# Optimization experiments

Hardware: AMD Instinct MI355X
Metric: run time of the kernel (lower is better)

Reference implementation:

```python
import jax, jax.numpy as jnp
import numpy as np

OUT, IN, GROUP = 4096, 4096, 128
NG = IN // GROUP  # 32 groups along in_features
TOKENS = 8192

def setup_inputs() -> dict:
    key = jax.random.key(0)
    k1, k2, k3, k4, k5 = jax.random.split(key, 5)
    input = jax.random.normal(k1, (TOKENS, IN), dtype=jnp.float32)
    qweight = jax.random.randint(k2, (OUT, IN), 0, 16, dtype=jnp.int32)
    scales = jax.random.uniform(k3, (OUT, NG), dtype=jnp.float32) * 0.02 + 0.001
    zeros = jax.random.uniform(k4, (OUT, NG), dtype=jnp.float32) * 15.0
    bias = jax.random.normal(k5, (OUT,), dtype=jnp.float32)
    return {"input": input, "qweight": qweight, "scales": scales, "zeros": zeros, "bias": bias}

def dequantize(qweight, scales, zeros):
    # qweight: [OUT, IN] int; scales/zeros: [OUT, NG]; group along in_features
    q = qweight.astype(jnp.float32).reshape(OUT, NG, GROUP)
    w = (q - zeros[:, :, None]) * scales[:, :, None]
    return w.reshape(OUT, IN)

def reference(input, qweight, scales, zeros, bias):
    # F.linear(input, W, bias) == input @ W.T + bias
    W = dequantize(qweight, scales, zeros)
    return jnp.einsum('ti,oi->to', input, W) + bias
```

## Files before the change

kernel.cpp:

```cpp
#include <hip/hip_runtime.h>
#include <hip/hip_bf16.h>
#include <cstdint>

typedef __attribute__((ext_vector_type(4))) float  floatx4;
typedef __attribute__((ext_vector_type(8))) __bf16 bf16x8;

#define M_T 8192
#define N_T 4096
#define K_T 4096
#define NG  32

__device__ __forceinline__ unsigned short f2bf(float f) {
    union { float f; unsigned int u; } v; v.f = f;
    unsigned int u = v.u;
    u += 0x7fffu + ((u >> 16) & 1u);
    return (unsigned short)(u >> 16);
}

__device__ __forceinline__ void load_lds16(const void* gsrc, void* ldst) {
    __builtin_amdgcn_global_load_lds(
        (const __attribute__((address_space(1))) uint32_t*)gsrc,
        (__attribute__((address_space(3))) uint32_t*)ldst,
        16, 0, 0);
}

__global__ void dequant_w_kernel(const int* __restrict__ q,
                                 const float* __restrict__ sc,
                                 const float* __restrict__ zr,
                                 unsigned short* __restrict__ Wb) {
    int idx = blockIdx.x * 256 + threadIdx.x;
    int e0 = idx << 2;
    int row = e0 >> 12;
    int col = e0 & 4095;
    int g = col >> 7;
    float s = sc[(row << 5) + g];
    float z = zr[(row << 5) + g];
    int4 qv = *(const int4*)(q + e0);
    ushort4 o;
    o.x = f2bf(((float)qv.x - z) * s);
    o.y = f2bf(((float)qv.y - z) * s);
    o.z = f2bf(((float)qv.z - z) * s);
    o.w = f2bf(((float)qv.w - z) * s);
    *(ushort4*)(Wb + e0) = o;
}

__global__ void convert_x_kernel(const float* __restrict__ X,
                                 unsigned short* __restrict__ Xb) {
    int idx = blockIdx.x * 256 + threadIdx.x;
    int e0 = idx << 2;
    float4 xv = *(const float4*)(X + e0);
    ushort4 o;
    o.x = f2bf(xv.x); o.y = f2bf(xv.y); o.z = f2bf(xv.z); o.w = f2bf(xv.w);
    *(ushort4*)(Xb + e0) = o;
}

__global__ __launch_bounds__(512, 2) void gemm256_8ph(
    const unsigned short* __restrict__ Xb,
    const unsigned short* __restrict__ Wb,
    const float* __restrict__ bias,
    float* __restrict__ C)
{
    __shared__ __align__(16) unsigned short lds[65536];
    char* ldsb = (char*)lds;

    const int tid  = threadIdx.x;
    const int lane = tid & 63;
    const int wid  = tid >> 6;
    const int wm   = wid >> 2;
    const int wn   = wid & 3;

    int bid = blockIdx.x;
    int xcd = bid & 7, r0 = bid >> 3;
    int mt = (xcd >> 1) * 8 + (r0 & 7);
    int nt = (xcd & 1) * 8 + (r0 >> 3);
    const int bm = mt * 256;
    const int bn = nt * 256;

    floatx4 acc[8][4] = {};

    const int klb = (lane >> 4) * 16;

    auto stage_half = [&](int buf, int isB, int half, int grow0, int k0,
                          const unsigned short* __restrict__ G) {
        char* base = ldsb + buf * 65536 + isB * 32768 + half * 16384;
        #pragma unroll
        for (int c = 0; c < 2; ++c) {
            int r  = c * 64 + wid * 8 + (lane >> 3);
            int cb = ((lane & 7) * 16) ^ ((lane >> 3) << 4);
            const char* src = (const char*)(G + (size_t)(grow0 + r) * K_T + k0) + cb;
            load_lds16(src, base + c * 8192 + wid * 1024);
        }
    };
    auto rdA = [&](int buf, int mf, int kb) -> bf16x8 {
        int r = mf * 16 + (lane & 15);
        int off = buf * 65536 + wm * 16384 + r * 128 + (kb ^ ((r & 7) << 4));
        return *(const bf16x8*)(ldsb + off);
    };
    auto rdB = [&](int buf, int nf, int kb) -> bf16x8 {
        int r = (wn & 1) * 64 + nf * 16 + (lane & 15);
        int off = buf * 65536 + 32768 + (wn >> 1) * 16384 + r * 128 + (kb ^ ((r & 7) << 4));
        return *(const bf16x8*)(ldsb + off);
    };

    stage_half(0, 1, 0, bn,       0,  Wb);
    stage_half(0, 1, 1, bn + 128, 0,  Wb);
    stage_half(0, 0, 0, bm,       0,  Xb);
    stage_half(0, 0, 1, bm + 128, 0,  Xb);
    stage_half(1, 1, 0, bn,       64, Wb);
    stage_half(1, 1, 1, bn + 128, 64, Wb);
    asm volatile("s_waitcnt vmcnt(4)" ::: "memory");
    __builtin_amdgcn_s_barrier();

    bf16x8 bfr[4][2];

    for (int t = 0; t < 32; ++t) {
        const int t1 = 2 * t + 1;
        const int t2 = (2 * t + 2 < 64) ? 2 * t + 2 : 63;
        const int t3 = (2 * t + 3 < 64) ? 2 * t + 3 : 63;
        #pragma unroll
        for (int p = 0; p < 8; ++p) {
            const int cb    = p >> 2;
            const int q     = p & 3;
            const int mbase = (q & 1) * 4;
            const int kkp   = q >> 1;

            if (q == 0) {
                #pragma unroll
                for (int nf = 0; nf < 4; ++nf)
                    bfr[nf][0] = rdB(cb, nf, klb);
            }
            if (q == 1) {
                #pragma unroll
                for (int nf = 0; nf < 4; ++nf)
                    bfr[nf][1] = rdB(cb, nf, 64 + klb);
            }
            bf16x8 a[4];
            #pragma unroll
            for (int m = 0; m < 4; ++m)
                a[m] = rdA(cb, mbase + m, kkp * 64 + klb);

            switch (p) {
                case 0: stage_half(1, 0, 0, bm,       t1 * 64, Xb); break;
                case 1: stage_half(1, 0, 1, bm + 128, t1 * 64, Xb); break;
                case 2: stage_half(0, 1, 0, bn,       t2 * 64, Wb); break;
                case 3: stage_half(0, 1, 1, bn + 128, t2 * 64, Wb); break;
                case 4: stage_half(0, 0, 0, bm,       t2 * 64, Xb); break;
                case 5: stage_half(0, 0, 1, bm + 128, t2 * 64, Xb); break;
                case 6: stage_half(1, 1, 0, bn,       t3 * 64, Wb); break;
                case 7: stage_half(1, 1, 1, bn + 128, t3 * 64, Wb); break;
            }

            __builtin_amdgcn_s_barrier();

            __builtin_amdgcn_s_setprio(1);
            #pragma unroll
            for (int m = 0; m < 4; ++m)
                #pragma unroll
                for (int nf = 0; nf < 4; ++nf)
                    acc[mbase + m][nf] = __builtin_amdgcn_mfma_f32_16x16x32_bf16(
                        a[m], bfr[nf][kkp], acc[mbase + m][nf], 0, 0, 0);
            __builtin_amdgcn_s_setprio(0);

            if (q == 1)
                asm volatile("s_waitcnt lgkmcnt(0)" ::: "memory");
            if (q == 3)
                asm volatile("s_waitcnt vmcnt(4)" ::: "memory");
            __builtin_amdgcn_s_barrier();
        }
    }

    asm volatile("s_waitcnt vmcnt(0)" ::: "memory");

    #pragma unroll
    for (int nf = 0; nf < 4; ++nf) {
        int col = bn + wn * 64 + nf * 16 + (lane & 15);
        float bv = bias[col];
        #pragma unroll
        for (int mf = 0; mf < 8; ++mf) {
            int row0 = bm + wm * 128 + mf * 16 + (lane >> 4) * 4;
            #pragma unroll
            for (int j = 0; j < 4; ++j)
                C[(size_t)(row0 + j) * N_T + col] = acc[mf][nf][j] + bv;
        }
    }
}

__global__ void fallback_gemm(const float* __restrict__ X,
                              const int* __restrict__ q,
                              const float* __restrict__ sc,
                              const float* __restrict__ zr,
                              const float* __restrict__ bias,
                              float* __restrict__ C) {
    __shared__ float sX[16][17];
    __shared__ float sW[16][17];
    int tx = threadIdx.x, ty = threadIdx.y;
    int row = blockIdx.y * 16 + ty;
    int col = blockIdx.x * 16 + tx;
    float acc = 0.f;
    for (int k0 = 0; k0 < K_T; k0 += 16) {
        sX[ty][tx] = X[(size_t)row * K_T + k0 + tx];
        int wrow = blockIdx.x * 16 + ty;
        int kc = k0 + tx;
        int g = kc >> 7;
        sW[ty][tx] = ((float)q[(size_t)wrow * K_T + kc] - zr[wrow * NG + g]) * sc[wrow * NG + g];
        __syncthreads();
        #pragma unroll
        for (int kk = 0; kk < 16; ++kk) acc += sX[ty][kk] * sW[tx][kk];
        __syncthreads();
    }
    C[(size_t)row * N_T + col] = acc + bias[col];
}

extern "C" void kernel_launch(void* const* d_in, const int* in_sizes, int n_in,
                              void* d_out, int out_size, void* d_ws, size_t ws_size,
                              hipStream_t stream) {
    const float* input   = (const float*)d_in[0];
    const int*   qweight = (const int*)d_in[1];
    const float* scales  = (const float*)d_in[2];
    const float* zeros   = (const float*)d_in[3];
    const float* bias    = (const float*)d_in[4];
    float* out = (float*)d_out;

    const size_t needW = (size_t)N_T * K_T * sizeof(unsigned short);
    const size_t needX = (size_t)M_T * K_T * sizeof(unsigned short);

    if (ws_size >= needW + needX) {
        unsigned short* Wb = (unsigned short*)d_ws;
        unsigned short* Xb = (unsigned short*)((char*)d_ws + needW);

        dequant_w_kernel<<<(N_T * K_T / 4) / 256, 256, 0, stream>>>(qweight, scales, zeros, Wb);
        convert_x_kernel<<<(M_T * K_T / 4) / 256, 256, 0, stream>>>(input, Xb);

        gemm256_8ph<<<512, 512, 0, stream>>>(Xb, Wb, bias, out);
    } else {
        dim3 blk(16, 16);
        dim3 grid(N_T / 16, M_T / 16);
        fallback_gemm<<<grid, blk, 0, stream>>>(input, qweight, scales, zeros, bias, out);
    }
}
```

Baseline: 284.9 us.

## Prefetch next-phase LDS fragments after MFMAs and drop mid-phase barrier

Precomputes per-lane LDS read offsets and global staging addresses so the inner loop uses constant-offset addressing. Moves the A and second-half B fragment reads to after each MFMA block, so LDS reads for the next phase overlap the current MFMA work. Removes the barrier between staging and compute in each phase, halving barriers per phase. This keeps more fragment registers live, and dropping the barrier relies on the remaining waitcnt and barrier placement still protecting the LDS buffers from being overwritten while in use.

```diff
diff --git a/kernel.cpp b/kernel.cpp
--- a/kernel.cpp
+++ b/kernel.cpp
@@ -78,40 +78,50 @@
 
     floatx4 acc[8][4] = {};
 
-    const int klb = (lane >> 4) * 16;
-
-    auto stage_half = [&](int buf, int isB, int half, int grow0, int k0,
-                          const unsigned short* __restrict__ G) {
-        char* base = ldsb + buf * 65536 + isB * 32768 + half * 16384;
-        #pragma unroll
-        for (int c = 0; c < 2; ++c) {
-            int r  = c * 64 + wid * 8 + (lane >> 3);
-            int cb = ((lane & 7) * 16) ^ ((lane >> 3) << 4);
-            const char* src = (const char*)(G + (size_t)(grow0 + r) * K_T + k0) + cb;
-            load_lds16(src, base + c * 8192 + wid * 1024);
+    const int klb  = (lane >> 4) * 16;
+    const int axor = (lane & 7) << 4;
+
+    int obA[2][2], obB[2][2];
+    #pragma unroll
+    for (int b = 0; b < 2; ++b)
+        #pragma unroll
+        for (int kp = 0; kp < 2; ++kp) {
+            obA[b][kp] = b * 65536 + wm * 16384 + (lane & 15) * 128
+                       + ((kp * 64 + klb) ^ axor);
+            obB[b][kp] = b * 65536 + 32768 + (wn >> 1) * 16384 + (wn & 1) * 8192
+                       + (lane & 15) * 128 + ((kp * 64 + klb) ^ axor);
         }
+
+    auto rA = [&](int b, int kp, int mf) -> bf16x8 {
+        return *(const bf16x8*)(ldsb + obA[b][kp] + mf * 2048);
     };
-    auto rdA = [&](int buf, int mf, int kb) -> bf16x8 {
-        int r = mf * 16 + (lane & 15);
-        int off = buf * 65536 + wm * 16384 + r * 128 + (kb ^ ((r & 7) << 4));
-        return *(const bf16x8*)(ldsb + off);
+    auto rB = [&](int b, int kp, int nf) -> bf16x8 {
+        return *(const bf16x8*)(ldsb + obB[b][kp] + nf * 2048);
     };
-    auto rdB = [&](int buf, int nf, int kb) -> bf16x8 {
-        int r = (wn & 1) * 64 + nf * 16 + (lane & 15);
-        int off = buf * 65536 + 32768 + (wn >> 1) * 16384 + r * 128 + (kb ^ ((r & 7) << 4));
-        return *(const bf16x8*)(ldsb + off);
+
+    const int pl0 = (wid * 8 + (lane >> 3)) * 8192
+                  + (((lane & 7) * 16) ^ ((lane >> 3) << 4));
+    const int pl1 = pl0 + 64 * 8192;
+    const char* GA = (const char*)Xb + (size_t)bm * 8192;
+    const char* GB = (const char*)Wb + (size_t)bn * 8192;
+
+    auto stage_half = [&](int buf, int isB, int half, int tk, const char* G) {
+        char* dst = ldsb + buf * 65536 + isB * 32768 + half * 16384 + wid * 1024;
+        const char* s0 = G + ((size_t)half * 1048576 + (size_t)tk * 128);
+        load_lds16(s0 + pl0, dst);
+        load_lds16(s0 + pl1, dst + 8192);
     };
 
-    stage_half(0, 1, 0, bn,       0,  Wb);
-    stage_half(0, 1, 1, bn + 128, 0,  Wb);
-    stage_half(0, 0, 0, bm,       0,  Xb);
-    stage_half(0, 0, 1, bm + 128, 0,  Xb);
-    stage_half(1, 1, 0, bn,       64, Wb);
-    stage_half(1, 1, 1, bn + 128, 64, Wb);
+    stage_half(0, 1, 0, 0, GB);
+    stage_half(0, 1, 1, 0, GB);
+    stage_half(0, 0, 0, 0, GA);
+    stage_half(0, 0, 1, 0, GA);
+    stage_half(1, 1, 0, 1, GB);
+    stage_half(1, 1, 1, 1, GB);
     asm volatile("s_waitcnt vmcnt(4)" ::: "memory");
     __builtin_amdgcn_s_barrier();
 
-    bf16x8 bfr[4][2];
+    bf16x8 a[4], bfr[4][2];
 
     for (int t = 0; t < 32; ++t) {
         const int t1 = 2 * t + 1;
@@ -121,36 +131,26 @@
         for (int p = 0; p < 8; ++p) {
             const int cb    = p >> 2;
             const int q     = p & 3;
+            const int kkp   = q >> 1;
             const int mbase = (q & 1) * 4;
-            const int kkp   = q >> 1;
 
             if (q == 0) {
                 #pragma unroll
-                for (int nf = 0; nf < 4; ++nf)
-                    bfr[nf][0] = rdB(cb, nf, klb);
-            }
-            if (q == 1) {
-                #pragma unroll
-                for (int nf = 0; nf < 4; ++nf)
-                    bfr[nf][1] = rdB(cb, nf, 64 + klb);
-            }
-            bf16x8 a[4];
-            #pragma unroll
-            for (int m = 0; m < 4; ++m)
-                a[m] = rdA(cb, mbase + m, kkp * 64 + klb);
+                for (int nf = 0; nf < 4; ++nf) bfr[nf][0] = rB(cb, 0, nf);
+                #pragma unroll
+                for (int m = 0; m < 4; ++m)    a[m] = rA(cb, 0, m);
+            }
 
             switch (p) {
-                case 0: stage_half(1, 0, 0, bm,       t1 * 64, Xb); break;
-                case 1: stage_half(1, 0, 1, bm + 128, t1 * 64, Xb); break;
-                case 2: stage_half(0, 1, 0, bn,       t2 * 64, Wb); break;
-                case 3: stage_half(0, 1, 1, bn + 128, t2 * 64, Wb); break;
-                case 4: stage_half(0, 0, 0, bm,       t2 * 64, Xb); break;
-                case 5: stage_half(0, 0, 1, bm + 128, t2 * 64, Xb); break;
-                case 6: stage_half(1, 1, 0, bn,       t3 * 64, Wb); break;
-                case 7: stage_half(1, 1, 1, bn + 128, t3 * 64, Wb); break;
-            }
-
-            __builtin_amdgcn_s_barrier();
+                case 0: stage_half(1, 0, 0, t1, GA); break;
+                case 1: stage_half(1, 0, 1, t1, GA); break;
+                case 2: stage_half(0, 1, 0, t2, GB); break;
+                case 3: stage_half(0, 1, 1, t2, GB); break;
+                case 4: stage_half(0, 0, 0, t2, GA); break;
+                case 5: stage_half(0, 0, 1, t2, GA); break;
+                case 6: stage_half(1, 1, 0, t3, GB); break;
+                case 7: stage_half(1, 1, 1, t3, GB); break;
+            }
 
             __builtin_amdgcn_s_setprio(1);
             #pragma unroll
@@ -160,6 +160,16 @@
                     acc[mbase + m][nf] = __builtin_amdgcn_mfma_f32_16x16x32_bf16(
                         a[m], bfr[nf][kkp], acc[mbase + m][nf], 0, 0, 0);
             __builtin_amdgcn_s_setprio(0);
+
+            if (q == 0) {
+                #pragma unroll
+                for (int nf = 0; nf < 4; ++nf) bfr[nf][1] = rB(cb, 1, nf);
+            }
+            if (q < 3) {
+                const int qn = q + 1, kkn = qn >> 1, mbn = (qn & 1) * 4;
+                #pragma unroll
+                for (int m = 0; m < 4; ++m) a[m] = rA(cb, kkn, mbn + m);
+            }
 
             if (q == 1)
                 asm volatile("s_waitcnt lgkmcnt(0)" ::: "memory");
```

After: 277.5 us. 2.6% less time.

## Restructure GEMM to 256x128 tiles with BK=32 triple-buffered LDS pipeline

Applied to the files above, without the earlier changes.

Replaces the 256x256-tile, 512-thread, BK=64 double-buffered GEMM with a 256x128-tile, 256-thread kernel using K-steps of 32 and a three-slot LDS ring. Loads run two tiles ahead and are split around the two MFMA halves, with a new XOR swizzle for 64-byte rows. The grid doubles to 1024 blocks with a remapped XCD tile assignment. The aim is smaller LDS use and finer-grained overlap of loads and MFMA, at the cost of more barriers per FLOP and more global traffic from the narrower N tile.

```diff
diff --git a/kernel.cpp b/kernel.cpp
--- a/kernel.cpp
+++ b/kernel.cpp
@@ -54,120 +54,111 @@
     *(ushort4*)(Xb + e0) = o;
 }
 
-__global__ __launch_bounds__(512, 2) void gemm256_8ph(
+__global__ __launch_bounds__(256, 2) void gemm_bk32(
     const unsigned short* __restrict__ Xb,
     const unsigned short* __restrict__ Wb,
     const float* __restrict__ bias,
     float* __restrict__ C)
 {
-    __shared__ __align__(16) unsigned short lds[65536];
+    __shared__ __align__(16) unsigned short lds[36864];
     char* ldsb = (char*)lds;
 
     const int tid  = threadIdx.x;
     const int lane = tid & 63;
     const int wid  = tid >> 6;
-    const int wm   = wid >> 2;
-    const int wn   = wid & 3;
+    const int wm   = wid >> 1;
+    const int wn   = wid & 1;
 
     int bid = blockIdx.x;
     int xcd = bid & 7, r0 = bid >> 3;
     int mt = (xcd >> 1) * 8 + (r0 & 7);
-    int nt = (xcd & 1) * 8 + (r0 >> 3);
+    int nt = (xcd & 1) * 16 + (r0 >> 3);
     const int bm = mt * 256;
-    const int bn = nt * 256;
+    const int bn = nt * 128;
 
     floatx4 acc[8][4] = {};
 
-    const int klb = (lane >> 4) * 16;
-
-    auto stage_half = [&](int buf, int isB, int half, int grow0, int k0,
-                          const unsigned short* __restrict__ G) {
-        char* base = ldsb + buf * 65536 + isB * 32768 + half * 16384;
-        #pragma unroll
-        for (int c = 0; c < 2; ++c) {
-            int r  = c * 64 + wid * 8 + (lane >> 3);
-            int cb = ((lane & 7) * 16) ^ ((lane >> 3) << 4);
-            const char* src = (const char*)(G + (size_t)(grow0 + r) * K_T + k0) + cb;
-            load_lds16(src, base + c * 8192 + wid * 1024);
-        }
-    };
-    auto rdA = [&](int buf, int mf, int kb) -> bf16x8 {
-        int r = mf * 16 + (lane & 15);
-        int off = buf * 65536 + wm * 16384 + r * 128 + (kb ^ ((r & 7) << 4));
-        return *(const bf16x8*)(ldsb + off);
-    };
-    auto rdB = [&](int buf, int nf, int kb) -> bf16x8 {
-        int r = (wn & 1) * 64 + nf * 16 + (lane & 15);
-        int off = buf * 65536 + 32768 + (wn >> 1) * 16384 + r * 128 + (kb ^ ((r & 7) << 4));
-        return *(const bf16x8*)(ldsb + off);
-    };
-
-    stage_half(0, 1, 0, bn,       0,  Wb);
-    stage_half(0, 1, 1, bn + 128, 0,  Wb);
-    stage_half(0, 0, 0, bm,       0,  Xb);
-    stage_half(0, 0, 1, bm + 128, 0,  Xb);
-    stage_half(1, 1, 0, bn,       64, Wb);
-    stage_half(1, 1, 1, bn + 128, 64, Wb);
-    asm volatile("s_waitcnt vmcnt(4)" ::: "memory");
+    const int l15 = lane & 15;
+    const int g   = lane >> 4;
+    const int obRead = l15 * 64 + 16 * (g ^ ((l15 >> 1) & 3));
+    const int obA_v  = obRead + wm * 8192;
+    const int obB_v  = 49152 + obRead + wn * 4096;
+
+    auto rA = [&](int sa, int mf) -> bf16x8 {
+        return *(const bf16x8*)(ldsb + obA_v + sa * 16384 + mf * 1024);
+    };
+    auto rB = [&](int sb, int nf) -> bf16x8 {
+        return *(const bf16x8*)(ldsb + obB_v + sb * 8192 + nf * 1024);
+    };
+
+    const int plS = (wid * 16 + (lane >> 2)) * 8192
+                  + 16 * ((lane & 3) ^ ((lane >> 3) & 3));
+    const char* GA = (const char*)Xb + (size_t)bm * 8192;
+    const char* GB = (const char*)Wb + (size_t)bn * 8192;
+
+    auto stA = [&](int slot, int tk, int c) {
+        load_lds16(GA + (size_t)tk * 64 + c * 524288 + plS,
+                   ldsb + slot * 16384 + c * 4096 + wid * 1024);
+    };
+    auto stB = [&](int slot, int tk, int c) {
+        load_lds16(GB + (size_t)tk * 64 + c * 524288 + plS,
+                   ldsb + 49152 + slot * 8192 + c * 4096 + wid * 1024);
+    };
+
+    stB(0, 0, 0); stB(0, 0, 1);
+    stA(0, 0, 0); stA(0, 0, 1); stA(0, 0, 2); stA(0, 0, 3);
+    stB(1, 1, 0); stB(1, 1, 1);
+    stA(1, 1, 0); stA(1, 1, 1); stA(1, 1, 2); stA(1, 1, 3);
+    asm volatile("s_waitcnt vmcnt(6)" ::: "memory");
     __builtin_amdgcn_s_barrier();
-
-    bf16x8 bfr[4][2];
-
-    for (int t = 0; t < 32; ++t) {
-        const int t1 = 2 * t + 1;
-        const int t2 = (2 * t + 2 < 64) ? 2 * t + 2 : 63;
-        const int t3 = (2 * t + 3 < 64) ? 2 * t + 3 : 63;
-        #pragma unroll
-        for (int p = 0; p < 8; ++p) {
-            const int cb    = p >> 2;
-            const int q     = p & 3;
-            const int mbase = (q & 1) * 4;
-            const int kkp   = q >> 1;
-
-            if (q == 0) {
-                #pragma unroll
-                for (int nf = 0; nf < 4; ++nf)
-                    bfr[nf][0] = rdB(cb, nf, klb);
-            }
-            if (q == 1) {
-                #pragma unroll
-                for (int nf = 0; nf < 4; ++nf)
-                    bfr[nf][1] = rdB(cb, nf, 64 + klb);
-            }
-            bf16x8 a[4];
+    asm volatile("" ::: "memory");
+
+    bf16x8 a[4], bfr[4];
+    #pragma unroll
+    for (int nf = 0; nf < 4; ++nf) bfr[nf] = rB(0, nf);
+    #pragma unroll
+    for (int m = 0; m < 4; ++m)    a[m] = rA(0, m);
+
+    auto tile_body = [&](int t, int sa, int sa1, int sa2) {
+        const int tk2 = (t + 2 < 128) ? t + 2 : 127;
+        stB(sa2, tk2, 0); stB(sa2, tk2, 1); stA(sa2, tk2, 0);
+        __builtin_amdgcn_s_setprio(1);
+        #pragma unroll
+        for (int m = 0; m < 4; ++m)
             #pragma unroll
-            for (int m = 0; m < 4; ++m)
-                a[m] = rdA(cb, mbase + m, kkp * 64 + klb);
-
-            switch (p) {
-                case 0: stage_half(1, 0, 0, bm,       t1 * 64, Xb); break;
-                case 1: stage_half(1, 0, 1, bm + 128, t1 * 64, Xb); break;
-                case 2: stage_half(0, 1, 0, bn,       t2 * 64, Wb); break;
-                case 3: stage_half(0, 1, 1, bn + 128, t2 * 64, Wb); break;
-                case 4: stage_half(0, 0, 0, bm,       t2 * 64, Xb); break;
-                case 5: stage_half(0, 0, 1, bm + 128, t2 * 64, Xb); break;
-                case 6: stage_half(1, 1, 0, bn,       t3 * 64, Wb); break;
-                case 7: stage_half(1, 1, 1, bn + 128, t3 * 64, Wb); break;
-            }
-
-            __builtin_amdgcn_s_barrier();
-
-            __builtin_amdgcn_s_setprio(1);
+            for (int nf = 0; nf < 4; ++nf)
+                acc[m][nf] = __builtin_amdgcn_mfma_f32_16x16x32_bf16(
+                    a[m], bfr[nf], acc[m][nf], 0, 0, 0);
+        __builtin_amdgcn_s_setprio(0);
+        #pragma unroll
+        for (int m = 0; m < 4; ++m) a[m] = rA(sa, 4 + m);
+        asm volatile("s_waitcnt vmcnt(3)" ::: "memory");
+        __builtin_amdgcn_s_barrier();
+        asm volatile("" ::: "memory");
+        stA(sa2, tk2, 1); stA(sa2, tk2, 2); stA(sa2, tk2, 3);
+        __builtin_amdgcn_s_setprio(1);
+        #pragma unroll
+        for (int m = 0; m < 4; ++m)
             #pragma unroll
-            for (int m = 0; m < 4; ++m)
-                #pragma unroll
-                for (int nf = 0; nf < 4; ++nf)
-                    acc[mbase + m][nf] = __builtin_amdgcn_mfma_f32_16x16x32_bf16(
-                        a[m], bfr[nf][kkp], acc[mbase + m][nf], 0, 0, 0);
-            __builtin_amdgcn_s_setprio(0);
-
-            if (q == 1)
-                asm volatile("s_waitcnt lgkmcnt(0)" ::: "memory");
-            if (q == 3)
-                asm volatile("s_waitcnt vmcnt(4)" ::: "memory");
-            __builtin_amdgcn_s_barrier();
-        }
-    }
+            for (int nf = 0; nf < 4; ++nf)
+                acc[4 + m][nf] = __builtin_amdgcn_mfma_f32_16x16x32_bf16(
+                    a[m], bfr[nf], acc[4 + m][nf], 0, 0, 0);
+        __builtin_amdgcn_s_setprio(0);
+        #pragma unroll
+        for (int nf = 0; nf < 4; ++nf) bfr[nf] = rB(sa1, nf);
+        #pragma unroll
+        for (int m = 0; m < 4; ++m)    a[m] = rA(sa1, m);
+        __builtin_amdgcn_s_barrier();
+        asm volatile("" ::: "memory");
+    };
+
+    for (int tb = 0; tb < 126; tb += 3) {
+        tile_body(tb,     0, 1, 2);
+        tile_body(tb + 1, 1, 2, 0);
+        tile_body(tb + 2, 2, 0, 1);
+    }
+    tile_body(126, 0, 1, 2);
+    tile_body(127, 1, 2, 0);
 
     asm volatile("s_waitcnt vmcnt(0)" ::: "memory");
 
@@ -231,7 +222,7 @@
         dequant_w_kernel<<<(N_T * K_T / 4) / 256, 256, 0, stream>>>(qweight, scales, zeros, Wb);
         convert_x_kernel<<<(M_T * K_T / 4) / 256, 256, 0, stream>>>(input, Xb);
 
-        gemm256_8ph<<<512, 512, 0, stream>>>(Xb, Wb, bias, out);
+        gemm_bk32<<<1024, 256, 0, stream>>>(Xb, Wb, bias, out);
     } else {
         dim3 blk(16, 16);
         dim3 grid(N_T / 16, M_T / 16);
```

Result: slower. 326.2 us (+14.5%).
